# Optimization experiments

Measured on AMD Instinct MI355X. Metric: run time of the kernel, lower is better.

## Reference

```python
import jax, jax.numpy as jnp
import numpy as np

H = 4          # n_head
DM = 512       # d_model
DK = 512       # d_k (hardcoded in module)
NL = 32        # num_landmarks
WS = 10        # window_size
EXT = WS // 2  # ext_len = 5
T = 2 * EXT + WS  # tile width = 20


def _ln(x, g, b, eps=1e-5):
    m = jnp.mean(x, axis=-1, keepdims=True)
    v = jnp.mean((x - m) ** 2, axis=-1, keepdims=True)
    return (x - m) / jnp.sqrt(v + eps) * g + b


def setup_inputs() -> dict:
    key = jax.random.key(0)
    ks = jax.random.split(key, 8)
    b, s = 8, 2000
    inp = {
        "X": jax.random.normal(ks[0], (b, s, DM), dtype=jnp.float32),
        "event_emb": jnp.zeros((1,), jnp.float32),
        "g": jnp.zeros((1,), jnp.float32),
        "mask": jnp.ones((b, s, 1), jnp.float32),
        "Wq": 0.02 * jax.random.normal(ks[1], (DM, H * DK), jnp.float32),
        "bq": jnp.zeros((H * DK,), jnp.float32),
        "Wk": 0.02 * jax.random.normal(ks[2], (DM, H * DK), jnp.float32),
        "bk": jnp.zeros((H * DK,), jnp.float32),
        "Wv": 0.02 * jax.random.normal(ks[3], (DM, H * DK), jnp.float32),
        "bv": jnp.zeros((H * DK,), jnp.float32),
        "Wo": 0.02 * jax.random.normal(ks[4], (H * DK, DM), jnp.float32),
        "bo": jnp.zeros((DM,), jnp.float32),
        "Wd": 0.02 * jax.random.normal(ks[5], (DM, H * NL), jnp.float32),
        "bd": jnp.zeros((H * NL,), jnp.float32),
        "lnl_g": jnp.ones((H * DK,), jnp.float32),
        "lnl_b": jnp.zeros((H * DK,), jnp.float32),
        "lns_g": jnp.ones((H * DK,), jnp.float32),
        "lns_b": jnp.zeros((H * DK,), jnp.float32),
    }
    return inp


def reference(X, event_emb, g, mask, Wq, bq, Wk, bk, Wv, bv, Wo, bo, Wd, bd,
              lnl_g, lnl_b, lns_g, lns_b):
    b, s, _ = X.shape
    G = s // WS  # number of windows
    scale = 1.0 / np.sqrt(DK)

    def split(x):  # [b,s,H*DK] -> [b,H,s,DK]
        return x.reshape(b, s, H, DK).transpose(0, 2, 1, 3)

    Q = split(X @ Wq + bq) * scale
    K = split(_ln(X @ Wk + bk, lnl_g, lnl_b))
    V = split(_ln(X @ Wv + bv, lnl_g, lnl_b))

    pad_mask = mask[..., 0] == 0  # [b,s] True where padded

    # landmark (Nystrom-style) compression
    hs = X @ Wd + bd  # [b,s,H*NL]
    hs = jnp.where(pad_mask[:, :, None], -jnp.inf, hs)
    hs = jax.nn.softmax(hs.astype(jnp.float32), axis=1).astype(X.dtype)
    hs = hs.reshape(b, s, H, NL).transpose(0, 2, 3, 1)  # [b,H,NL,s]
    K_c = jnp.einsum('bhls,bhsd->bhld', hs, K)  # [b,H,NL,DK]
    V_c = jnp.einsum('bhls,bhsd->bhld', hs, V)
    # dual_ln_s over flattened heads
    K_c = _ln(K_c.transpose(0, 2, 1, 3).reshape(b, NL, H * DK), lns_g, lns_b)
    K_c = K_c.reshape(b, NL, H, DK).transpose(0, 2, 1, 3)
    V_c = _ln(V_c.transpose(0, 2, 1, 3).reshape(b, NL, H * DK), lns_g, lns_b)
    V_c = V_c.reshape(b, NL, H, DK).transpose(0, 2, 1, 3)

    attn_compress = jnp.einsum('bhsd,bhld->bhsl', Q, K_c)  # [b,H,s,NL]

    # sliding-window chunked attention (v2 tiling)
    idx = jnp.arange(G)[:, None] * WS + jnp.arange(T)[None, :]  # [G,T]
    K_pad = jnp.pad(K, ((0, 0), (0, 0), (EXT, EXT), (0, 0)))
    K_tiles = K_pad[:, :, idx, :]  # [b,H,G,T,DK]
    m_pad = jnp.pad(pad_mask, ((0, 0), (EXT, EXT)), constant_values=True)
    m_tiles = m_pad[:, idx]  # [b,G,T]
    Q_tiles = Q.reshape(b, H, G, WS, DK)
    win = jnp.einsum('bhgwd,bhgtd->bhgwt', Q_tiles, K_tiles)  # [b,H,G,WS,T]
    win = jnp.where(m_tiles[:, None, :, None, :], -jnp.inf, win)
    win = win.reshape(b, H, s, T)

    scores = jnp.concatenate([attn_compress, win], axis=-1)  # [b,H,s,NL+T]
    attn = jax.nn.softmax(scores.astype(jnp.float32), axis=-1).astype(X.dtype)
    attn = jnp.where(pad_mask[:, None, :, None], 0.0, attn)

    C = jnp.einsum('bhsl,bhld->bhsd', attn[..., :NL], V_c)
    V_pad = jnp.pad(V, ((0, 0), (0, 0), (EXT, EXT), (0, 0)))
    V_tiles = V_pad[:, :, idx, :]  # [b,H,G,T,DK]
    win_p = attn[..., NL:].reshape(b, H, G, WS, T)
    C = C + jnp.einsum('bhgwt,bhgtd->bhgwd', win_p, V_tiles).reshape(b, H, s, DK)

    out = C.transpose(0, 2, 1, 3).reshape(b, s, H * DK) @ Wo + bo
    return out
```

## Files before the change

### kernel.cpp

```cpp
#include <hip/hip_runtime.h>
#include <math.h>

#define BB 8
#define SS 2000
#define DMM 512
#define HHN 4
#define DKK 512
#define HDK 2048
#define NLL 32
#define HNL 128
#define GGN 200
#define WSZ 10
#define TTN 20
#define EXTT 5
#define MMR (BB*SS)

typedef unsigned short bf16_t;
typedef __attribute__((ext_vector_type(8))) short short8;
typedef __attribute__((ext_vector_type(4))) float floatx4;

__device__ __forceinline__ float bf2f(bf16_t u) {
  union { unsigned u; float f; } x; x.u = ((unsigned)u) << 16; return x.f;
}
__device__ __forceinline__ bf16_t f2bf(float f) {
  union { float f; unsigned u; } x; x.f = f;
  unsigned r = x.u + 0x7FFFu + ((x.u >> 16) & 1u);
  return (bf16_t)(r >> 16);
}

__device__ __forceinline__ float block_sum256(float v, float* sh) {
  #pragma unroll
  for (int off = 32; off > 0; off >>= 1) v += __shfl_down(v, off);
  if ((threadIdx.x & 63) == 0) sh[threadIdx.x >> 6] = v;
  __syncthreads();
  float t = sh[0] + sh[1] + sh[2] + sh[3];
  __syncthreads();
  return t;
}

__global__ __launch_bounds__(256)
void transpose_w(const float* __restrict__ W, bf16_t* __restrict__ Wt,
                 int K, int N) {
  __shared__ float Ts[64][65];
  int n0 = blockIdx.x * 64, k0 = blockIdx.y * 64;
  int tid = threadIdx.x;
  #pragma unroll
  for (int i = 0; i < 16; ++i) {
    int e = i * 256 + tid;
    int r = e >> 6, c = e & 63;
    Ts[r][c] = W[(size_t)(k0 + r) * N + n0 + c];
  }
  __syncthreads();
  #pragma unroll
  for (int i = 0; i < 16; ++i) {
    int e = i * 256 + tid;
    int r = e >> 6, c = e & 63;
    Wt[(size_t)(n0 + r) * K + k0 + c] = f2bf(Ts[c][r]);
  }
}

template <typename TA, typename TO>
__global__ __launch_bounds__(256)
void gemm_mfma(const TA* __restrict__ A, const bf16_t* __restrict__ Bt,
               const float* __restrict__ bias, TO* __restrict__ Cout,
               int M, int N, int K, float alpha) {
  __shared__ bf16_t As[128 * 32];
  __shared__ bf16_t Bs[128 * 32];
  int tid = threadIdx.x;
  int wave = tid >> 6, lane = tid & 63;
  int wr = wave >> 1, wc = wave & 1;
  int quad = lane >> 4, ml = lane & 15;
  int bm = blockIdx.y * 128, bn = blockIdx.x * 128;

  floatx4 acc[4][4];
  #pragma unroll
  for (int i = 0; i < 4; ++i)
    #pragma unroll
    for (int j = 0; j < 4; ++j)
      #pragma unroll
      for (int r = 0; r < 4; ++r) acc[i][j][r] = 0.f;

  for (int k0 = 0; k0 < K; k0 += 32) {
    #pragma unroll
    for (int p = 0; p < 2; ++p) {
      int idx = p * 256 + tid;
      int row = idx >> 2, ch = idx & 3;
      int sw = ch ^ (row & 3);
      if constexpr (sizeof(TA) == 4) {
        float4 a0 = *(const float4*)&A[(size_t)(bm + row) * K + k0 + ch * 8];
        float4 a1 = *(const float4*)&A[(size_t)(bm + row) * K + k0 + ch * 8 + 4];
        ushort4 u0, u1;
        u0.x = f2bf(a0.x); u0.y = f2bf(a0.y); u0.z = f2bf(a0.z); u0.w = f2bf(a0.w);
        u1.x = f2bf(a1.x); u1.y = f2bf(a1.y); u1.z = f2bf(a1.z); u1.w = f2bf(a1.w);
        *(ushort4*)&As[row * 32 + sw * 8]     = u0;
        *(ushort4*)&As[row * 32 + sw * 8 + 4] = u1;
      } else {
        uint4 raw = *(const uint4*)&A[(size_t)(bm + row) * K + k0 + ch * 8];
        *(uint4*)&As[row * 32 + sw * 8] = raw;
      }
      uint4 braw = *(const uint4*)&Bt[(size_t)(bn + row) * K + k0 + ch * 8];
      *(uint4*)&Bs[row * 32 + sw * 8] = braw;
    }
    __syncthreads();
    short8 af[4], bfr[4];
    #pragma unroll
    for (int i = 0; i < 4; ++i) {
      int row = wr * 64 + i * 16 + ml;
      int sw = quad ^ (row & 3);
      af[i] = *(const short8*)&As[row * 32 + sw * 8];
    }
    #pragma unroll
    for (int j = 0; j < 4; ++j) {
      int row = wc * 64 + j * 16 + ml;
      int sw = quad ^ (row & 3);
      bfr[j] = *(const short8*)&Bs[row * 32 + sw * 8];
    }
    #pragma unroll
    for (int i = 0; i < 4; ++i)
      #pragma unroll
      for (int j = 0; j < 4; ++j)
        acc[i][j] = __builtin_amdgcn_mfma_f32_16x16x32_bf16(af[i], bfr[j], acc[i][j], 0, 0, 0);
    __syncthreads();
  }
  #pragma unroll
  for (int i = 0; i < 4; ++i) {
    int row0 = bm + wr * 64 + i * 16 + quad * 4;
    #pragma unroll
    for (int j = 0; j < 4; ++j) {
      int col = bn + wc * 64 + j * 16 + ml;
      float bv = bias[col];
      #pragma unroll
      for (int r = 0; r < 4; ++r) {
        float o = (acc[i][j][r] + bv) * alpha;
        if constexpr (sizeof(TO) == 2)
          Cout[(size_t)(row0 + r) * N + col] = f2bf(o);
        else
          Cout[(size_t)(row0 + r) * N + col] = o;
      }
    }
  }
}

__global__ __launch_bounds__(256)
void ln2048_bf16(bf16_t* __restrict__ Y, const float* __restrict__ gam,
                 const float* __restrict__ bet) {
  __shared__ float sh[4];
  bf16_t* y = Y + (size_t)blockIdx.x * HDK;
  int t = threadIdx.x;
  ushort4 ra = *(const ushort4*)&y[t * 8];
  ushort4 rb = *(const ushort4*)&y[t * 8 + 4];
  float v[8];
  v[0] = bf2f(ra.x); v[1] = bf2f(ra.y); v[2] = bf2f(ra.z); v[3] = bf2f(ra.w);
  v[4] = bf2f(rb.x); v[5] = bf2f(rb.y); v[6] = bf2f(rb.z); v[7] = bf2f(rb.w);
  float s = 0.f;
  #pragma unroll
  for (int j = 0; j < 8; ++j) s += v[j];
  s = block_sum256(s, sh);
  float mean = s * (1.f / 2048.f);
  float ss = 0.f;
  #pragma unroll
  for (int j = 0; j < 8; ++j) { float d = v[j] - mean; ss = fmaf(d, d, ss); }
  ss = block_sum256(ss, sh);
  float rstd = rsqrtf(ss * (1.f / 2048.f) + 1e-5f);
  float gg[8], bb[8];
  *(float4*)&gg[0] = *(const float4*)&gam[t * 8];
  *(float4*)&gg[4] = *(const float4*)&gam[t * 8 + 4];
  *(float4*)&bb[0] = *(const float4*)&bet[t * 8];
  *(float4*)&bb[4] = *(const float4*)&bet[t * 8 + 4];
  ushort4 oa, ob;
  oa.x = f2bf((v[0] - mean) * rstd * gg[0] + bb[0]);
  oa.y = f2bf((v[1] - mean) * rstd * gg[1] + bb[1]);
  oa.z = f2bf((v[2] - mean) * rstd * gg[2] + bb[2]);
  oa.w = f2bf((v[3] - mean) * rstd * gg[3] + bb[3]);
  ob.x = f2bf((v[4] - mean) * rstd * gg[4] + bb[4]);
  ob.y = f2bf((v[5] - mean) * rstd * gg[5] + bb[5]);
  ob.z = f2bf((v[6] - mean) * rstd * gg[6] + bb[6]);
  ob.w = f2bf((v[7] - mean) * rstd * gg[7] + bb[7]);
  *(ushort4*)&y[t * 8] = oa;
  *(ushort4*)&y[t * 8 + 4] = ob;
}

__global__ __launch_bounds__(256)
void hs_colsum(const float* __restrict__ hs, const float* __restrict__ mask,
               float* __restrict__ Ssum) {
  __shared__ float red[128];
  int b = blockIdx.x / 100;
  int chunk = blockIdx.x % 100;
  int tid = threadIdx.x;
  int c = tid & 127, half = tid >> 7;
  int s0 = chunk * 20;
  float sum = 0.f;
  #pragma unroll
  for (int i = 0; i < 10; ++i) {
    int s = s0 + i * 2 + half;
    float m = mask[(size_t)b * SS + s];
    float v = hs[((size_t)b * SS + s) * HNL + c];
    sum += (m != 0.f) ? __expf(v) : 0.f;
  }
  if (half == 1) red[c] = sum;
  __syncthreads();
  if (half == 0) atomicAdd(&Ssum[b * HNL + c], sum + red[c]);
}

__global__ __launch_bounds__(256)
void compress_mfma(const bf16_t* __restrict__ Kf, const bf16_t* __restrict__ Vf,
                   const float* __restrict__ hs, const float* __restrict__ mask,
                   const float* __restrict__ Ssum, float* __restrict__ Kc,
                   float* __restrict__ Vc) {
  int dch = blockIdx.x & 3;
  int sch = (blockIdx.x >> 2) & 7;
  int bh  = blockIdx.x >> 5;
  int h = bh & 3, b = bh >> 2;
  int sbase = sch * 250;
  int dbase = dch * 128;

  __shared__ __align__(16) bf16_t Ah[32 * 40];
  __shared__ __align__(16) bf16_t Kt[128 * 40];
  __shared__ __align__(16) bf16_t Vt[128 * 40];

  int tid = threadIdx.x;
  int wave = tid >> 6, lane = tid & 63;
  int tensor = wave >> 1, nh = wave & 1;
  int quad = lane >> 4, ml = lane & 15;

  float inv8[8];
  if (tid < 128) {
    int l0 = (tid & 3) * 8;
    #pragma unroll
    for (int j = 0; j < 8; ++j)
      inv8[j] = 1.f / Ssum[b * HNL + h * NLL + l0 + j];
  }

  floatx4 acc[2][4];
  #pragma unroll
  for (int i = 0; i < 2; ++i)
    #pragma unroll
    for (int j = 0; j < 4; ++j)
      #pragma unroll
      for (int r = 0; r < 4; ++r) acc[i][j][r] = 0.f;

  for (int ks = 0; ks < 8; ++ks) {
    int s0 = ks * 32;
    if (tid < 128) {
      int si = tid >> 2;
      int l0 = (tid & 3) * 8;
      int s_l = s0 + si;
      float w[8];
      #pragma unroll
      for (int j = 0; j < 8; ++j) w[j] = 0.f;
      if (s_l < 250) {
        float m = mask[(size_t)b * SS + sbase + s_l];
        if (m != 0.f) {
          const float* p = &hs[((size_t)b * SS + sbase + s_l) * HNL + h * NLL + l0];
          float4 f0 = *(const float4*)p;
          float4 f1 = *(const float4*)(p + 4);
          w[0] = __expf(f0.x) * inv8[0];
          w[1] = __expf(f0.y) * inv8[1];
          w[2] = __expf(f0.z) * inv8[2];
          w[3] = __expf(f0.w) * inv8[3];
          w[4] = __expf(f1.x) * inv8[4];
          w[5] = __expf(f1.y) * inv8[5];
          w[6] = __expf(f1.z) * inv8[6];
          w[7] = __expf(f1.w) * inv8[7];
        }
      }
      #pragma unroll
      for (int j = 0; j < 8; ++j)
        Ah[(l0 + j) * 40 + si] = f2bf(w[j]);
    }
    {
      int si = tid >> 3;
      int d0 = (tid & 7) * 16;
      int s_l = s0 + si;
      uint4 ka = {0, 0, 0, 0}, kb = {0, 0, 0, 0};
      uint4 va = {0, 0, 0, 0}, vb = {0, 0, 0, 0};
      if (s_l < 250) {
        size_t gof = ((size_t)b * SS + sbase + s_l) * HDK + h * DKK + dbase + d0;
        ka = *(const uint4*)&Kf[gof];
        kb = *(const uint4*)&Kf[gof + 8];
        va = *(const uint4*)&Vf[gof];
        vb = *(const uint4*)&Vf[gof + 8];
      }
      const ushort* kp = (const ushort*)&ka;
      const ushort* kq = (const ushort*)&kb;
      const ushort* vp = (const ushort*)&va;
      const ushort* vq = (const ushort*)&vb;
      #pragma unroll
      for (int j = 0; j < 8; ++j) {
        Kt[(d0 + j) * 40 + si]     = kp[j];
        Kt[(d0 + 8 + j) * 40 + si] = kq[j];
        Vt[(d0 + j) * 40 + si]     = vp[j];
        Vt[(d0 + 8 + j) * 40 + si] = vq[j];
      }
    }
    __syncthreads();
    const bf16_t* Bsel = tensor ? Vt : Kt;
    #pragma unroll
    for (int i = 0; i < 2; ++i) {
      short8 af = *(const short8*)&Ah[(i * 16 + ml) * 40 + quad * 8];
      #pragma unroll
      for (int j = 0; j < 4; ++j) {
        short8 bfr = *(const short8*)&Bsel[(nh * 64 + j * 16 + ml) * 40 + quad * 8];
        acc[i][j] = __builtin_amdgcn_mfma_f32_16x16x32_bf16(af, bfr, acc[i][j], 0, 0, 0);
      }
    }
    __syncthreads();
  }
  float* outp = tensor ? Vc : Kc;
  size_t obase = ((size_t)b * 4 + h) * (NLL * DKK);
  #pragma unroll
  for (int i = 0; i < 2; ++i) {
    #pragma unroll
    for (int j = 0; j < 4; ++j) {
      int d = dbase + nh * 64 + j * 16 + ml;
      #pragma unroll
      for (int r = 0; r < 4; ++r) {
        int l = i * 16 + quad * 4 + r;
        atomicAdd(&outp[obase + (size_t)l * DKK + d], acc[i][j][r]);
      }
    }
  }
}

__global__ __launch_bounds__(256)
void ln_comp_out(const float* __restrict__ Y, const float* __restrict__ gam,
                 const float* __restrict__ bet, bf16_t* __restrict__ outp,
                 int transposed) {
  __shared__ float sh[4];
  int b = blockIdx.x >> 5, l = blockIdx.x & 31;
  size_t base = (size_t)b * 65536 + (size_t)l * 512;
  float v[8]; float s = 0.f;
  #pragma unroll
  for (int j = 0; j < 8; ++j) {
    int f = threadIdx.x + 256 * j;
    int hh = f >> 9, dd = f & 511;
    v[j] = Y[base + (size_t)hh * 16384 + dd];
    s += v[j];
  }
  s = block_sum256(s, sh);
  float mean = s * (1.f / 2048.f);
  float ss = 0.f;
  #pragma unroll
  for (int j = 0; j < 8; ++j) { float d = v[j] - mean; ss = fmaf(d, d, ss); }
  ss = block_sum256(ss, sh);
  float rstd = rsqrtf(ss * (1.f / 2048.f) + 1e-5f);
  #pragma unroll
  for (int j = 0; j < 8; ++j) {
    int f = threadIdx.x + 256 * j;
    int hh = f >> 9, dd = f & 511;
    float o = (v[j] - mean) * rstd * gam[f] + bet[f];
    if (!transposed)
      outp[(((size_t)b * 4 + hh) * 32 + l) * 512 + dd] = f2bf(o);
    else
      outp[(((size_t)b * 4 + hh) * 512 + dd) * 32 + l] = f2bf(o);
  }
}

__global__ __launch_bounds__(256)
void attn_mfma3(const bf16_t* __restrict__ Qf, const bf16_t* __restrict__ Kf,
                const bf16_t* __restrict__ Vf, const bf16_t* __restrict__ KcB,
                const bf16_t* __restrict__ VcT, const float* __restrict__ mask,
                bf16_t* __restrict__ Cf) {
  int gp = blockIdx.x % 100;
  int bh = blockIdx.x / 100;
  int h = bh & 3, b = bh >> 2;
  int g0row = gp * 20;
  int wbase = g0row - EXTT;

  __shared__ bf16_t VwT[128 * 40];
  __shared__ bf16_t Vst[30 * 136];
  __shared__ float  sc[20][68];
  __shared__ bf16_t Ps[32 * 88];
  __shared__ float  cv[32];

  int tid = threadIdx.x;
  int wave = tid >> 6, lane = tid & 63;
  int quad = lane >> 4, ml = lane & 15;

  if (tid < 30) {
    int j = wbase + tid;
    cv[tid] = (j >= 0 && j < SS && mask[(size_t)b * SS + j] != 0.f) ? 1.f : 0.f;
  }
  for (int i = tid; i < 32 * 88; i += 256) Ps[i] = 0;

  int qr0 = g0row + (ml < 20 ? ml : 19);
  int r1c = 16 + ml;
  int qr1 = g0row + (r1c < 20 ? r1c : 19);
  const bf16_t* ap0 = Qf + ((size_t)b * SS + qr0) * HDK + h * DKK;
  const bf16_t* ap1 = Qf + ((size_t)b * SS + qr1) * HDK + h * DKK;
  int brow = wave * 16 + ml;
  const bf16_t* bp;
  if (brow < 32) {
    bp = KcB + ((size_t)bh * 32 + brow) * 512;
  } else {
    int j = wbase + brow - 32;
    j = j < 0 ? 0 : (j >= SS ? SS - 1 : j);
    bp = Kf + ((size_t)b * SS + j) * HDK + h * DKK;
  }
  floatx4 s0 = {0.f, 0.f, 0.f, 0.f}, s1 = {0.f, 0.f, 0.f, 0.f};
  #pragma unroll 8
  for (int ks = 0; ks < 16; ++ks) {
    short8 af0 = *(const short8*)(ap0 + ks * 32 + quad * 8);
    short8 af1 = *(const short8*)(ap1 + ks * 32 + quad * 8);
    short8 bfr = *(const short8*)(bp  + ks * 32 + quad * 8);
    s0 = __builtin_amdgcn_mfma_f32_16x16x32_bf16(af0, bfr, s0, 0, 0, 0);
    s1 = __builtin_amdgcn_mfma_f32_16x16x32_bf16(af1, bfr, s1, 0, 0, 0);
  }
  #pragma unroll
  for (int r = 0; r < 4; ++r) {
    int row0 = quad * 4 + r;
    if (row0 < 20) sc[row0][wave * 16 + ml] = s0[r];
    int row1 = 16 + quad * 4 + r;
    if (row1 < 20) sc[row1][wave * 16 + ml] = s1[r];
  }

  uint4 vr[2];
  #pragma unroll
  for (int vi = 0; vi < 2; ++vi) {
    int idx = vi * 256 + tid;
    uint4 z = {0, 0, 0, 0};
    if (idx < 480) {
      int u = idx >> 4, c8 = idx & 15;
      int j = wbase + u;
      if (j >= 0 && j < SS)
        z = *(const uint4*)&Vf[((size_t)b * SS + j) * HDK + h * DKK + c8 * 8];
    }
    vr[vi] = z;
  }
  __syncthreads();

  if (tid < 160) {
    int r = tid >> 3, part = tid & 7;
    float mx = -INFINITY;
    #pragma unroll
    for (int i = 0; i < 8; ++i) {
      int c = part + i * 8;
      if (c < 62) {
        float v = sc[r][c];
        bool valid;
        if (c < 32) valid = true;
        else {
          int u = c - 32;
          valid = (u < 30) && (cv[u] != 0.f) && (r < 10 ? (u < 20) : (u >= 10));
        }
        v = valid ? v : -INFINITY;
        sc[r][c] = v;
        mx = fmaxf(mx, v);
      }
    }
    mx = fmaxf(mx, __shfl_xor(mx, 1));
    mx = fmaxf(mx, __shfl_xor(mx, 2));
    mx = fmaxf(mx, __shfl_xor(mx, 4));
    float sum = 0.f;
    #pragma unroll
    for (int i = 0; i < 8; ++i) {
      int c = part + i * 8;
      if (c < 62) {
        float e = expf(sc[r][c] - mx);
        sc[r][c] = e;
        sum += e;
      }
    }
    sum += __shfl_xor(sum, 1);
    sum += __shfl_xor(sum, 2);
    sum += __shfl_xor(sum, 4);
    float qm = mask[(size_t)b * SS + g0row + r];
    float inv = (qm != 0.f) ? 1.f / sum : 0.f;
    #pragma unroll
    for (int i = 0; i < 8; ++i) {
      int c = part + i * 8;
      if (c < 62) {
        float p = sc[r][c] * inv;
        if (c < 32) Ps[r * 88 + c] = f2bf(p);
        else        Ps[r * 88 + 40 + (c - 32)] = f2bf(p);
      }
    }
  }
  #pragma unroll
  for (int vi = 0; vi < 2; ++vi) {
    int idx = vi * 256 + tid;
    if (idx < 480) {
      int u = idx >> 4, c8 = idx & 15;
      *(uint4*)&Vst[u * 136 + c8 * 8] = vr[vi];
    }
  }
  __syncthreads();

  short8 pac0 = *(const short8*)&Ps[ml * 88 + quad * 8];
  short8 pac1 = *(const short8*)&Ps[(16 + ml) * 88 + quad * 8];
  short8 paw0 = *(const short8*)&Ps[ml * 88 + 40 + quad * 8];
  short8 paw1 = *(const short8*)&Ps[(16 + ml) * 88 + 40 + quad * 8];
  size_t vctbase = ((size_t)bh * 512) * 32;
  size_t cbase = ((size_t)b * SS + g0row) * HDK + h * DKK;

  #pragma unroll
  for (int ch = 0; ch < 4; ++ch) {
    int dA = ch * 128 + (wave * 2 + 0) * 16 + ml;
    int dB = ch * 128 + (wave * 2 + 1) * 16 + ml;
    short8 vcfA = *(const short8*)&VcT[vctbase + (size_t)dA * 32 + quad * 8];
    short8 vcfB = *(const short8*)&VcT[vctbase + (size_t)dB * 32 + quad * 8];
    if (ch < 3) {
      #pragma unroll
      for (int vi = 0; vi < 2; ++vi) {
        int idx = vi * 256 + tid;
        uint4 z = {0, 0, 0, 0};
        if (idx < 480) {
          int u = idx >> 4, c8 = idx & 15;
          int j = wbase + u;
          if (j >= 0 && j < SS)
            z = *(const uint4*)&Vf[((size_t)b * SS + j) * HDK + h * DKK + (ch + 1) * 128 + c8 * 8];
        }
        vr[vi] = z;
      }
    }
    #pragma unroll
    for (int g = 0; g < 16; ++g) {
      int gid = g * 4 + wave;
      int d0 = (gid & 7) * 16, u0 = (gid >> 3) * 4;
      int u = u0 + quad, dl = d0 + ml;
      bf16_t v = (u < 30) ? Vst[u * 136 + dl] : (bf16_t)0;
      VwT[dl * 40 + u] = v;
    }
    __syncthreads();

    #pragma unroll
    for (int half = 0; half < 2; ++half) {
      int d = ch * 128 + (wave * 2 + half) * 16 + ml;
      int dl = d - ch * 128;
      short8 vcf = half ? vcfB : vcfA;
      short8 vwf = *(const short8*)&VwT[dl * 40 + quad * 8];
      floatx4 o0 = {0.f, 0.f, 0.f, 0.f}, o1 = {0.f, 0.f, 0.f, 0.f};
      o0 = __builtin_amdgcn_mfma_f32_16x16x32_bf16(pac0, vcf, o0, 0, 0, 0);
      o0 = __builtin_amdgcn_mfma_f32_16x16x32_bf16(paw0, vwf, o0, 0, 0, 0);
      o1 = __builtin_amdgcn_mfma_f32_16x16x32_bf16(pac1, vcf, o1, 0, 0, 0);
      o1 = __builtin_amdgcn_mfma_f32_16x16x32_bf16(paw1, vwf, o1, 0, 0, 0);
      #pragma unroll
      for (int r = 0; r < 4; ++r) {
        int row0 = quad * 4 + r;
        if (row0 < 20) Cf[cbase + (size_t)row0 * HDK + d] = f2bf(o0[r]);
        int row1 = 16 + quad * 4 + r;
        if (row1 < 20) Cf[cbase + (size_t)row1 * HDK + d] = f2bf(o1[r]);
      }
    }
    if (ch < 3) {
      #pragma unroll
      for (int vi = 0; vi < 2; ++vi) {
        int idx = vi * 256 + tid;
        if (idx < 480) {
          int u = idx >> 4, c8 = idx & 15;
          *(uint4*)&Vst[u * 136 + c8 * 8] = vr[vi];
        }
      }
    }
    __syncthreads();
  }
}

extern "C" void kernel_launch(void* const* d_in, const int* in_sizes, int n_in,
                              void* d_out, int out_size, void* d_ws, size_t ws_size,
                              hipStream_t stream) {
  const float* X     = (const float*)d_in[0];
  const float* mask  = (const float*)d_in[3];
  const float* Wq    = (const float*)d_in[4];
  const float* bq    = (const float*)d_in[5];
  const float* Wk    = (const float*)d_in[6];
  const float* bk    = (const float*)d_in[7];
  const float* Wv    = (const float*)d_in[8];
  const float* bv    = (const float*)d_in[9];
  const float* Wo    = (const float*)d_in[10];
  const float* bo    = (const float*)d_in[11];
  const float* Wd    = (const float*)d_in[12];
  const float* bd    = (const float*)d_in[13];
  const float* lnl_g = (const float*)d_in[14];
  const float* lnl_b = (const float*)d_in[15];
  const float* lns_g = (const float*)d_in[16];
  const float* lns_b = (const float*)d_in[17];
  float* out = (float*)d_out;

  char* ws = (char*)d_ws;
  bf16_t* Q   = (bf16_t*)(ws);
  bf16_t* K   = (bf16_t*)(ws + 65536000);
  bf16_t* V   = (bf16_t*)(ws + 131072000);
  float*  hs  = (float*) (ws + 196608000);
  float*  Kc  = (float*) (ws + 204800000);
  float*  Vc  = (float*) (ws + 206897152);
  bf16_t* C   = Q;
  bf16_t* Wqt = (bf16_t*)(ws + 196608000);
  bf16_t* Wkt = (bf16_t*)(ws + 196608000 + 2097152);
  bf16_t* Wvt = (bf16_t*)(ws + 196608000 + 4194304);
  bf16_t* Wdt = (bf16_t*)(ws + 204800000);
  bf16_t* Wot = (bf16_t*)(ws + 65536000);
  bf16_t* KcB = (bf16_t*)(ws + 196608000);
  bf16_t* VcT = (bf16_t*)(ws + 196608000 + 1048576);
  float* Ssum = (float*)d_out;

  const float scale = 0.04419417382415922f;
  const dim3 blk(256);

  transpose_w<<<dim3(32, 8), blk, 0, stream>>>(Wq, Wqt, 512, 2048);
  transpose_w<<<dim3(32, 8), blk, 0, stream>>>(Wk, Wkt, 512, 2048);
  transpose_w<<<dim3(32, 8), blk, 0, stream>>>(Wv, Wvt, 512, 2048);
  transpose_w<<<dim3(2, 8),  blk, 0, stream>>>(Wd, Wdt, 512, 128);
  gemm_mfma<float, bf16_t><<<dim3(16, 125), blk, 0, stream>>>(X, Wqt, bq, Q, MMR, 2048, 512, scale);
  gemm_mfma<float, bf16_t><<<dim3(16, 125), blk, 0, stream>>>(X, Wkt, bk, K, MMR, 2048, 512, 1.f);
  gemm_mfma<float, bf16_t><<<dim3(16, 125), blk, 0, stream>>>(X, Wvt, bv, V, MMR, 2048, 512, 1.f);
  gemm_mfma<float, float ><<<dim3(1, 125),  blk, 0, stream>>>(X, Wdt, bd, hs, MMR, 128, 512, 1.f);
  hipMemsetAsync(d_out, 0, BB * HNL * sizeof(float), stream);
  ln2048_bf16<<<MMR, blk, 0, stream>>>(K, lnl_g, lnl_b);
  ln2048_bf16<<<MMR, blk, 0, stream>>>(V, lnl_g, lnl_b);
  hs_colsum<<<BB * 100, blk, 0, stream>>>(hs, mask, Ssum);
  hipMemsetAsync(ws + 204800000, 0, 4194304, stream);
  compress_mfma<<<1024, blk, 0, stream>>>(K, V, hs, mask, Ssum, Kc, Vc);
  ln_comp_out<<<BB * NLL, blk, 0, stream>>>(Kc, lns_g, lns_b, KcB, 0);
  ln_comp_out<<<BB * NLL, blk, 0, stream>>>(Vc, lns_g, lns_b, VcT, 1);
  attn_mfma3<<<BB * HHN * 100, blk, 0, stream>>>(Q, K, V, KcB, VcT, mask, C);
  transpose_w<<<dim3(8, 32), blk, 0, stream>>>(Wo, Wot, 2048, 512);
  gemm_mfma<bf16_t, float><<<dim3(4, 125), blk, 0, stream>>>(C, Wot, bo, out, MMR, 512, 2048, 1.f);
}
```

Baseline: 612.5 us.

## Pre-convert X to bf16, fuse QKV GEMMs, use direct global-to-LDS loads

Adds a one-off kernel that converts X to bf16 into spare output memory, so the projection GEMMs no longer each load fp32 X and convert it inside the k-loop. The three Q/K/V projections are merged into one launch over the concatenated transposed weights, with per-block selection of bias, scale and destination. All GEMMs now stage tiles through global_load_lds with the XOR swizzle applied on the global-address side, which removes register round-trips. The cost is an extra conversion pass and a dependence on the compiler placing the right waits before the barrier.

Measured after the change: 535.5 us. 12.6% less time.

```diff
diff --git a/kernel.cpp b/kernel.cpp
--- a/kernel.cpp
+++ b/kernel.cpp
@@ -19,6 +19,10 @@
 typedef __attribute__((ext_vector_type(8))) short short8;
 typedef __attribute__((ext_vector_type(4))) float floatx4;
 
+#define GLL16(gp, lp) __builtin_amdgcn_global_load_lds( \
+    (__attribute__((address_space(1))) void*)(gp), \
+    (__attribute__((address_space(3))) void*)(lp), 16, 0, 0)
+
 __device__ __forceinline__ float bf2f(bf16_t u) {
   union { unsigned u; float f; } x; x.u = ((unsigned)u) << 16; return x.f;
 }
@@ -39,6 +43,18 @@
 }
 
 __global__ __launch_bounds__(256)
+void x_to_bf16(const float* __restrict__ X, bf16_t* __restrict__ Xb) {
+  int i = blockIdx.x * 256 + threadIdx.x;
+  float4 a = *(const float4*)&X[(size_t)i * 8];
+  float4 b = *(const float4*)&X[(size_t)i * 8 + 4];
+  ushort4 u0, u1;
+  u0.x = f2bf(a.x); u0.y = f2bf(a.y); u0.z = f2bf(a.z); u0.w = f2bf(a.w);
+  u1.x = f2bf(b.x); u1.y = f2bf(b.y); u1.z = f2bf(b.z); u1.w = f2bf(b.w);
+  *(ushort4*)&Xb[(size_t)i * 8] = u0;
+  *(ushort4*)&Xb[(size_t)i * 8 + 4] = u1;
+}
+
+__global__ __launch_bounds__(256)
 void transpose_w(const float* __restrict__ W, bf16_t* __restrict__ Wt,
                  int K, int N) {
   __shared__ float Ts[64][65];
@@ -59,9 +75,9 @@
   }
 }
 
-template <typename TA, typename TO>
-__global__ __launch_bounds__(256)
-void gemm_mfma(const TA* __restrict__ A, const bf16_t* __restrict__ Bt,
+template <typename TO>
+__global__ __launch_bounds__(256)
+void gemm_bf16(const bf16_t* __restrict__ A, const bf16_t* __restrict__ Bt,
                const float* __restrict__ bias, TO* __restrict__ Cout,
                int M, int N, int K, float alpha) {
   __shared__ bf16_t As[128 * 32];
@@ -80,27 +96,20 @@
       #pragma unroll
       for (int r = 0; r < 4; ++r) acc[i][j][r] = 0.f;
 
+  int lin0 = wave * 64 + lane;
+  int lin1 = 256 + lin0;
+  int row0 = lin0 >> 2, ch0 = (lin0 & 3) ^ (row0 & 3);
+  int row1 = lin1 >> 2, ch1 = (lin1 & 3) ^ (row1 & 3);
+  const bf16_t* gA0 = &A[(size_t)(bm + row0) * K + ch0 * 8];
+  const bf16_t* gA1 = &A[(size_t)(bm + row1) * K + ch1 * 8];
+  const bf16_t* gB0 = &Bt[(size_t)(bn + row0) * K + ch0 * 8];
+  const bf16_t* gB1 = &Bt[(size_t)(bn + row1) * K + ch1 * 8];
+
   for (int k0 = 0; k0 < K; k0 += 32) {
-    #pragma unroll
-    for (int p = 0; p < 2; ++p) {
-      int idx = p * 256 + tid;
-      int row = idx >> 2, ch = idx & 3;
-      int sw = ch ^ (row & 3);
-      if constexpr (sizeof(TA) == 4) {
-        float4 a0 = *(const float4*)&A[(size_t)(bm + row) * K + k0 + ch * 8];
-        float4 a1 = *(const float4*)&A[(size_t)(bm + row) * K + k0 + ch * 8 + 4];
-        ushort4 u0, u1;
-        u0.x = f2bf(a0.x); u0.y = f2bf(a0.y); u0.z = f2bf(a0.z); u0.w = f2bf(a0.w);
-        u1.x = f2bf(a1.x); u1.y = f2bf(a1.y); u1.z = f2bf(a1.z); u1.w = f2bf(a1.w);
-        *(ushort4*)&As[row * 32 + sw * 8]     = u0;
-        *(ushort4*)&As[row * 32 + sw * 8 + 4] = u1;
-      } else {
-        uint4 raw = *(const uint4*)&A[(size_t)(bm + row) * K + k0 + ch * 8];
-        *(uint4*)&As[row * 32 + sw * 8] = raw;
-      }
-      uint4 braw = *(const uint4*)&Bt[(size_t)(bn + row) * K + k0 + ch * 8];
-      *(uint4*)&Bs[row * 32 + sw * 8] = braw;
-    }
+    GLL16(gA0 + k0, &As[lin0 * 8]);
+    GLL16(gA1 + k0, &As[lin1 * 8]);
+    GLL16(gB0 + k0, &Bs[lin0 * 8]);
+    GLL16(gB1 + k0, &Bs[lin1 * 8]);
     __syncthreads();
     short8 af[4], bfr[4];
     #pragma unroll
@@ -124,7 +133,7 @@
   }
   #pragma unroll
   for (int i = 0; i < 4; ++i) {
-    int row0 = bm + wr * 64 + i * 16 + quad * 4;
+    int row0o = bm + wr * 64 + i * 16 + quad * 4;
     #pragma unroll
     for (int j = 0; j < 4; ++j) {
       int col = bn + wc * 64 + j * 16 + ml;
@@ -133,9 +142,87 @@
       for (int r = 0; r < 4; ++r) {
         float o = (acc[i][j][r] + bv) * alpha;
         if constexpr (sizeof(TO) == 2)
-          Cout[(size_t)(row0 + r) * N + col] = f2bf(o);
+          Cout[(size_t)(row0o + r) * N + col] = f2bf(o);
         else
-          Cout[(size_t)(row0 + r) * N + col] = o;
+          Cout[(size_t)(row0o + r) * N + col] = o;
+      }
+    }
+  }
+}
+
+__global__ __launch_bounds__(256)
+void gemm_qkv(const bf16_t* __restrict__ A, const bf16_t* __restrict__ Bt,
+              const float* __restrict__ bq, const float* __restrict__ bk,
+              const float* __restrict__ bv, bf16_t* __restrict__ Qo,
+              bf16_t* __restrict__ Ko, bf16_t* __restrict__ Vo, float scale) {
+  const int K = 512;
+  __shared__ bf16_t As[128 * 32];
+  __shared__ bf16_t Bs[128 * 32];
+  int tid = threadIdx.x;
+  int wave = tid >> 6, lane = tid & 63;
+  int wr = wave >> 1, wc = wave & 1;
+  int quad = lane >> 4, ml = lane & 15;
+  int bm = blockIdx.y * 128, bn = blockIdx.x * 128;
+  int nb = bn >> 11;
+  const float* bias = nb == 0 ? bq : (nb == 1 ? bk : bv);
+  bf16_t* Cout = nb == 0 ? Qo : (nb == 1 ? Ko : Vo);
+  float alpha = nb == 0 ? scale : 1.f;
+  int bcol = bn & 2047;
+
+  floatx4 acc[4][4];
+  #pragma unroll
+  for (int i = 0; i < 4; ++i)
+    #pragma unroll
+    for (int j = 0; j < 4; ++j)
+      #pragma unroll
+      for (int r = 0; r < 4; ++r) acc[i][j][r] = 0.f;
+
+  int lin0 = wave * 64 + lane;
+  int lin1 = 256 + lin0;
+  int row0 = lin0 >> 2, ch0 = (lin0 & 3) ^ (row0 & 3);
+  int row1 = lin1 >> 2, ch1 = (lin1 & 3) ^ (row1 & 3);
+  const bf16_t* gA0 = &A[(size_t)(bm + row0) * K + ch0 * 8];
+  const bf16_t* gA1 = &A[(size_t)(bm + row1) * K + ch1 * 8];
+  const bf16_t* gB0 = &Bt[(size_t)(bn + row0) * K + ch0 * 8];
+  const bf16_t* gB1 = &Bt[(size_t)(bn + row1) * K + ch1 * 8];
+
+  for (int k0 = 0; k0 < K; k0 += 32) {
+    GLL16(gA0 + k0, &As[lin0 * 8]);
+    GLL16(gA1 + k0, &As[lin1 * 8]);
+    GLL16(gB0 + k0, &Bs[lin0 * 8]);
+    GLL16(gB1 + k0, &Bs[lin1 * 8]);
+    __syncthreads();
+    short8 af[4], bfr[4];
+    #pragma unroll
+    for (int i = 0; i < 4; ++i) {
+      int row = wr * 64 + i * 16 + ml;
+      int sw = quad ^ (row & 3);
+      af[i] = *(const short8*)&As[row * 32 + sw * 8];
+    }
+    #pragma unroll
+    for (int j = 0; j < 4; ++j) {
+      int row = wc * 64 + j * 16 + ml;
+      int sw = quad ^ (row & 3);
+      bfr[j] = *(const short8*)&Bs[row * 32 + sw * 8];
+    }
+    #pragma unroll
+    for (int i = 0; i < 4; ++i)
+      #pragma unroll
+      for (int j = 0; j < 4; ++j)
+        acc[i][j] = __builtin_amdgcn_mfma_f32_16x16x32_bf16(af[i], bfr[j], acc[i][j], 0, 0, 0);
+    __syncthreads();
+  }
+  #pragma unroll
+  for (int i = 0; i < 4; ++i) {
+    int row0o = bm + wr * 64 + i * 16 + quad * 4;
+    #pragma unroll
+    for (int j = 0; j < 4; ++j) {
+      int col = bcol + wc * 64 + j * 16 + ml;
+      float bv2 = bias[col];
+      #pragma unroll
+      for (int r = 0; r < 4; ++r) {
+        float o = (acc[i][j][r] + bv2) * alpha;
+        Cout[(size_t)(row0o + r) * HDK + col] = f2bf(o);
       }
     }
   }
@@ -592,19 +679,19 @@
   bf16_t* Wot = (bf16_t*)(ws + 65536000);
   bf16_t* KcB = (bf16_t*)(ws + 196608000);
   bf16_t* VcT = (bf16_t*)(ws + 196608000 + 1048576);
-  float* Ssum = (float*)d_out;
+  float*  Ssum = (float*)d_out;
+  bf16_t* Xbf  = (bf16_t*)((char*)d_out + 65536);
 
   const float scale = 0.04419417382415922f;
   const dim3 blk(256);
 
+  x_to_bf16<<<4000, blk, 0, stream>>>(X, Xbf);
   transpose_w<<<dim3(32, 8), blk, 0, stream>>>(Wq, Wqt, 512, 2048);
   transpose_w<<<dim3(32, 8), blk, 0, stream>>>(Wk, Wkt, 512, 2048);
   transpose_w<<<dim3(32, 8), blk, 0, stream>>>(Wv, Wvt, 512, 2048);
   transpose_w<<<dim3(2, 8),  blk, 0, stream>>>(Wd, Wdt, 512, 128);
-  gemm_mfma<float, bf16_t><<<dim3(16, 125), blk, 0, stream>>>(X, Wqt, bq, Q, MMR, 2048, 512, scale);
-  gemm_mfma<float, bf16_t><<<dim3(16, 125), blk, 0, stream>>>(X, Wkt, bk, K, MMR, 2048, 512, 1.f);
-  gemm_mfma<float, bf16_t><<<dim3(16, 125), blk, 0, stream>>>(X, Wvt, bv, V, MMR, 2048, 512, 1.f);
-  gemm_mfma<float, float ><<<dim3(1, 125),  blk, 0, stream>>>(X, Wdt, bd, hs, MMR, 128, 512, 1.f);
+  gemm_qkv<<<dim3(48, 125), blk, 0, stream>>>(Xbf, Wqt, bq, bk, bv, Q, K, V, scale);
+  gemm_bf16<float><<<dim3(1, 125), blk, 0, stream>>>(Xbf, Wdt, bd, hs, MMR, 128, 512, 1.f);
   hipMemsetAsync(d_out, 0, BB * HNL * sizeof(float), stream);
   ln2048_bf16<<<MMR, blk, 0, stream>>>(K, lnl_g, lnl_b);
   ln2048_bf16<<<MMR, blk, 0, stream>>>(V, lnl_g, lnl_b);
@@ -615,5 +702,5 @@
   ln_comp_out<<<BB * NLL, blk, 0, stream>>>(Vc, lns_g, lns_b, VcT, 1);
   attn_mfma3<<<BB * HHN * 100, blk, 0, stream>>>(Q, K, V, KcB, VcT, mask, C);
   transpose_w<<<dim3(8, 32), blk, 0, stream>>>(Wo, Wot, 2048, 512);
-  gemm_mfma<bf16_t, float><<<dim3(4, 125), blk, 0, stream>>>(C, Wot, bo, out, MMR, 512, 2048, 1.f);
-}
+  gemm_bf16<float><<<dim3(4, 125), blk, 0, stream>>>(C, Wot, bo, out, MMR, 512, 2048, 1.f);
+}
```
